# Kernel optimization log

Measured on AMD Instinct MI355X. Metric: run time of the kernel, lower is better.

Reference implementation:

```python
import jax, jax.numpy as jnp
import numpy as np

BATCH = 256
INPUT_DIM = 64
LEVELS = 100
HV_DIM = 10000


def setup_inputs() -> dict:
    key = jax.random.key(0)
    kx, kb = jax.random.split(key)
    x = jax.random.uniform(kx, (BATCH, INPUT_DIM), dtype=jnp.float32)
    base = jax.random.normal(kb, (INPUT_DIM, LEVELS, HV_DIM), dtype=jnp.float32)
    # buffer is L2-normalized along hv_dim at construction time
    base = base / jnp.linalg.norm(base, axis=-1, keepdims=True)
    return {"x": x, "base_hvs": base}


def reference(x, base_hvs):
    D, L, H = base_hvs.shape
    B = x.shape[0]
    xn = jnp.clip(x * (L - 1), 0.0, float(L - 1))          # [B, D]
    lo = jnp.floor(xn).astype(jnp.int32)                    # [B, D]
    hi = jnp.clip(lo + 1, 0, L - 1)                         # [B, D]
    alpha = xn - lo.astype(x.dtype)                         # [B, D]

    def step(acc, inputs):
        bhv, l, h, a = inputs    # bhv: [L, H], l/h/a: [B]
        hv_low = bhv[l]          # [B, H] gather
        hv_high = bhv[h]         # [B, H] gather
        a = a[:, None]
        return acc + (1.0 - a) * hv_low + a * hv_high, None

    init = jnp.zeros((B, H), dtype=x.dtype)
    encoded, _ = jax.lax.scan(step, init, (base_hvs, lo.T, hi.T, alpha.T))
    return encoded / jnp.linalg.norm(encoded, axis=-1, keepdims=True)
```

## Files before the change

### kernel.cpp

```cpp
#include <hip/hip_runtime.h>
#include <hip/hip_fp16.h>
#include <hip/hip_bf16.h>

#define BATCH   256
#define DIMS    64
#define LEVELS  100
#define HVD     10000
#define WH      64
#define NHT     157
#define DSPLIT  8
#define DPER    8
#define TPB     256
#define CHUNK_FLOATS (LEVELS * WH)
#define NSTG    25

typedef unsigned int   uint;
typedef unsigned short ushort;

#define PRM_OFF_BYTES (DSPLIT * BATCH * HVD * 2)

static __device__ __forceinline__ ushort f2bf(float f) {
    __hip_bfloat16 h = __float2bfloat16(f);
    return *reinterpret_cast<ushort*>(&h);
}

__global__ __launch_bounds__(256) void setup_kernel(
    const float* __restrict__ x, uint* __restrict__ prm)
{
    const int i = blockIdx.x * 256 + threadIdx.x;
    if (i >= DIMS * BATCH) return;
    const int d = i >> 8;
    const int b = i & 255;
    float xv = x[b * DIMS + d];
    float xn = fminf(fmaxf(xv * (float)(LEVELS - 1), 0.0f), (float)(LEVELS - 1));
    float fl = floorf(xn);
    int   lo = (int)fl;
    int   hi = lo < LEVELS - 1 ? lo + 1 : LEVELS - 1;
    uint abits = (uint)__half_as_ushort(__float2half(xn - fl));
    prm[i] = abits | ((uint)lo << 16) | ((uint)hi << 24);
}

__global__ __launch_bounds__(TPB, 2) void encode_kernel(
    const float* __restrict__ base,
    const uint* __restrict__ prm,
    ushort*     __restrict__ partial)
{
    __shared__ float s_buf[2][CHUNK_FLOATS];
    __shared__ uint  s_prm[DPER][BATCH];

    const int tid   = threadIdx.x;
    const int w     = tid >> 6;
    const int lane  = tid & 63;
    const int htile = blockIdx.x;
    const int split = blockIdx.y;
    const int h0    = htile * WH;
    const int d0    = split * DPER;
    const int wvalid = (HVD - h0) < WH ? (HVD - h0) : WH;

    {
        const uint4* pg = (const uint4*)(prm + d0 * BATCH);
        uint4* pl = (uint4*)&s_prm[0][0];
        for (int i = tid; i < DPER * BATCH / 4; i += TPB) pl[i] = pg[i];
    }
    __syncthreads();

    const int srow = lane >> 4;
    const int scol = (lane & 15) * 4;
    const float* srcdim = base + (size_t)d0 * LEVELS * HVD + h0;

    auto issue_chunk = [&](int dc, int bufidx) {
        const float* src = srcdim + (size_t)dc * LEVELS * HVD;
        float* dst = &s_buf[bufidx][0];
        for (int p = w; p < NSTG; p += 4) {
            const float* g = src + (size_t)(4 * p + srow) * HVD + scol;
            if (scol < wvalid) {
                __builtin_amdgcn_global_load_lds(
                    (const __attribute__((address_space(1))) uint*)g,
                    (__attribute__((address_space(3))) uint*)(dst + p * 4 * WH),
                    16, 0, 0);
            }
        }
    };

    issue_chunk(0, 0);
    issue_chunk(1, 1);

    const int sub   = lane >> 5;
    const int p2    = lane & 31;
    const int pb    = p2 * 8;
    const int bbase = w * 64;

    float2 acc[32];
    #pragma unroll
    for (int j = 0; j < 32; ++j) acc[j] = make_float2(0.f, 0.f);

    #pragma unroll 1
    for (int dc = 0; dc < DPER; ++dc) {
        if (dc < DPER - 1) asm volatile("s_waitcnt vmcnt(6)" ::: "memory");
        else               asm volatile("s_waitcnt vmcnt(0)" ::: "memory");
        __builtin_amdgcn_s_barrier();

        const char* buf = (const char*)&s_buf[dc & 1][0];
        #pragma unroll
        for (int j = 0; j < 32; ++j) {
            uint2 pp = *(const uint2*)&s_prm[dc][bbase + 2 * j];
            const uint pk = sub ? pp.y : pp.x;
            const float a = __half2float(__ushort_as_half((ushort)(pk & 0xffffu)));
            const int olo = (int)((pk >> 16) & 0xffu) << 8;
            const int ohi = (int)(pk >> 24) << 8;
            const float2 vlo = *(const float2*)(buf + olo + pb);
            const float2 vhi = *(const float2*)(buf + ohi + pb);
            const float wl = 1.0f - a;
            acc[j].x += wl * vlo.x + a * vhi.x;
            acc[j].y += wl * vlo.y + a * vhi.y;
        }
        asm volatile("" ::: "memory");
        __builtin_amdgcn_s_barrier();
        if (dc < DPER - 2) issue_chunk(dc + 2, dc & 1);
    }

    if (p2 * 2 < wvalid) {
        #pragma unroll
        for (int j = 0; j < 32; ++j) {
            const int b = bbase + 2 * j + sub;
            const uint pk = (uint)f2bf(acc[j].x) | ((uint)f2bf(acc[j].y) << 16);
            *(uint*)(partial + ((size_t)split * BATCH + b) * (size_t)HVD + h0 + p2 * 2) = pk;
        }
    }
}

__global__ __launch_bounds__(256) void finish_kernel(
    const ushort* __restrict__ partial,
    float* __restrict__ out)
{
    const int b   = blockIdx.x;
    const int tid = threadIdx.x;

    float ss = 0.f;
    for (int i = tid; i < HVD / 4; i += 256) {
        float4 sum = make_float4(0.f, 0.f, 0.f, 0.f);
        #pragma unroll
        for (int sp = 0; sp < DSPLIT; ++sp) {
            const uint2 u = *(const uint2*)(partial +
                ((size_t)sp * BATCH + b) * (size_t)HVD + i * 4);
            sum.x += __uint_as_float(u.x << 16);
            sum.y += __uint_as_float(u.x & 0xffff0000u);
            sum.z += __uint_as_float(u.y << 16);
            sum.w += __uint_as_float(u.y & 0xffff0000u);
        }
        *(float4*)(out + (size_t)b * HVD + i * 4) = sum;
        ss += sum.x * sum.x + sum.y * sum.y + sum.z * sum.z + sum.w * sum.w;
    }

    __shared__ float red[256];
    red[tid] = ss;
    __syncthreads();
    #pragma unroll
    for (int sh = 128; sh > 0; sh >>= 1) {
        if (tid < sh) red[tid] += red[tid + sh];
        __syncthreads();
    }
    const float inv = rsqrtf(red[0]);

    for (int i = tid; i < HVD / 4; i += 256) {
        float4 v = *(float4*)(out + (size_t)b * HVD + i * 4);
        v.x *= inv; v.y *= inv; v.z *= inv; v.w *= inv;
        *(float4*)(out + (size_t)b * HVD + i * 4) = v;
    }
}

extern "C" void kernel_launch(void* const* d_in, const int* in_sizes, int n_in,
                              void* d_out, int out_size, void* d_ws, size_t ws_size,
                              hipStream_t stream)
{
    const float* x    = (const float*)d_in[0];
    const float* base = (const float*)d_in[1];
    float*       out  = (float*)d_out;
    ushort*      part = (ushort*)d_ws;
    uint*        prm  = (uint*)((char*)d_ws + PRM_OFF_BYTES);

    setup_kernel<<<DIMS, 256, 0, stream>>>(x, prm);
    dim3 grid(NHT, DSPLIT);
    encode_kernel<<<grid, TPB, 0, stream>>>(base, prm, part);
    finish_kernel<<<BATCH, 256, 0, stream>>>(part, out);
}
```

Baseline: 381.4 us.

## Fuse parameter setup into encode kernel and keep finish results in registers

Removes the separate setup kernel: each encode block now computes the lo/hi/alpha parameters for its 8 dims directly from x into shared memory, saving one launch and a global round trip. The finish kernel switches to 1024 threads, each handling 8 elements held in registers, so the output is written once after normalization instead of being written, reread and rewritten. The cost is redundant parameter computation across the 157 h-tiles and a larger reduction tree in finish.

```diff
diff --git a/kernel.cpp b/kernel.cpp
--- a/kernel.cpp
+++ b/kernel.cpp
@@ -11,38 +11,22 @@
 #define DSPLIT  8
 #define DPER    8
 #define TPB     256
+#define FTPB    1024
 #define CHUNK_FLOATS (LEVELS * WH)
 #define NSTG    25
 
 typedef unsigned int   uint;
 typedef unsigned short ushort;
 
-#define PRM_OFF_BYTES (DSPLIT * BATCH * HVD * 2)
 
 static __device__ __forceinline__ ushort f2bf(float f) {
     __hip_bfloat16 h = __float2bfloat16(f);
     return *reinterpret_cast<ushort*>(&h);
 }
 
-__global__ __launch_bounds__(256) void setup_kernel(
-    const float* __restrict__ x, uint* __restrict__ prm)
-{
-    const int i = blockIdx.x * 256 + threadIdx.x;
-    if (i >= DIMS * BATCH) return;
-    const int d = i >> 8;
-    const int b = i & 255;
-    float xv = x[b * DIMS + d];
-    float xn = fminf(fmaxf(xv * (float)(LEVELS - 1), 0.0f), (float)(LEVELS - 1));
-    float fl = floorf(xn);
-    int   lo = (int)fl;
-    int   hi = lo < LEVELS - 1 ? lo + 1 : LEVELS - 1;
-    uint abits = (uint)__half_as_ushort(__float2half(xn - fl));
-    prm[i] = abits | ((uint)lo << 16) | ((uint)hi << 24);
-}
-
 __global__ __launch_bounds__(TPB, 2) void encode_kernel(
+    const float* __restrict__ x,
     const float* __restrict__ base,
-    const uint* __restrict__ prm,
     ushort*     __restrict__ partial)
 {
     __shared__ float s_buf[2][CHUNK_FLOATS];
@@ -58,9 +42,20 @@
     const int wvalid = (HVD - h0) < WH ? (HVD - h0) : WH;
 
     {
-        const uint4* pg = (const uint4*)(prm + d0 * BATCH);
-        uint4* pl = (uint4*)&s_prm[0][0];
-        for (int i = tid; i < DPER * BATCH / 4; i += TPB) pl[i] = pg[i];
+        const float4* xr = (const float4*)(x + (size_t)tid * DIMS + d0);
+        const float4 xa = xr[0];
+        const float4 xb = xr[1];
+        const float xv[8] = { xa.x, xa.y, xa.z, xa.w, xb.x, xb.y, xb.z, xb.w };
+        #pragma unroll
+        for (int k = 0; k < DPER; ++k) {
+            float xn = fminf(fmaxf(xv[k] * (float)(LEVELS - 1), 0.0f),
+                             (float)(LEVELS - 1));
+            float fl = floorf(xn);
+            int   lo = (int)fl;
+            int   hi = lo < LEVELS - 1 ? lo + 1 : LEVELS - 1;
+            uint abits = (uint)__half_as_ushort(__float2half(xn - fl));
+            s_prm[k][tid] = abits | ((uint)lo << 16) | ((uint)hi << 24);
+        }
     }
     __syncthreads();
 
@@ -129,43 +124,60 @@
     }
 }
 
-__global__ __launch_bounds__(256) void finish_kernel(
+__global__ __launch_bounds__(FTPB) void finish_kernel(
     const ushort* __restrict__ partial,
     float* __restrict__ out)
 {
     const int b   = blockIdx.x;
     const int tid = threadIdx.x;
 
-    float ss = 0.f;
-    for (int i = tid; i < HVD / 4; i += 256) {
-        float4 sum = make_float4(0.f, 0.f, 0.f, 0.f);
-        #pragma unroll
-        for (int sp = 0; sp < DSPLIT; ++sp) {
-            const uint2 u = *(const uint2*)(partial +
-                ((size_t)sp * BATCH + b) * (size_t)HVD + i * 4);
-            sum.x += __uint_as_float(u.x << 16);
-            sum.y += __uint_as_float(u.x & 0xffff0000u);
-            sum.z += __uint_as_float(u.y << 16);
-            sum.w += __uint_as_float(u.y & 0xffff0000u);
+    float4 v0[2], v1[2];
+    float  ss = 0.f;
+    #pragma unroll
+    for (int k = 0; k < 2; ++k) {
+        const int g = k * FTPB + tid;
+        float4 a = make_float4(0.f, 0.f, 0.f, 0.f);
+        float4 c = make_float4(0.f, 0.f, 0.f, 0.f);
+        if (g < HVD / 8) {
+            #pragma unroll
+            for (int sp = 0; sp < DSPLIT; ++sp) {
+                const uint4 u = *(const uint4*)(partial +
+                    ((size_t)sp * BATCH + b) * (size_t)HVD + (size_t)g * 8);
+                a.x += __uint_as_float(u.x << 16);
+                a.y += __uint_as_float(u.x & 0xffff0000u);
+                a.z += __uint_as_float(u.y << 16);
+                a.w += __uint_as_float(u.y & 0xffff0000u);
+                c.x += __uint_as_float(u.z << 16);
+                c.y += __uint_as_float(u.z & 0xffff0000u);
+                c.z += __uint_as_float(u.w << 16);
+                c.w += __uint_as_float(u.w & 0xffff0000u);
+            }
+            ss += a.x * a.x + a.y * a.y + a.z * a.z + a.w * a.w
+                + c.x * c.x + c.y * c.y + c.z * c.z + c.w * c.w;
         }
-        *(float4*)(out + (size_t)b * HVD + i * 4) = sum;
-        ss += sum.x * sum.x + sum.y * sum.y + sum.z * sum.z + sum.w * sum.w;
+        v0[k] = a; v1[k] = c;
     }
 
-    __shared__ float red[256];
+    __shared__ float red[FTPB];
     red[tid] = ss;
     __syncthreads();
     #pragma unroll
-    for (int sh = 128; sh > 0; sh >>= 1) {
+    for (int sh = FTPB / 2; sh > 0; sh >>= 1) {
         if (tid < sh) red[tid] += red[tid + sh];
         __syncthreads();
     }
     const float inv = rsqrtf(red[0]);
 
-    for (int i = tid; i < HVD / 4; i += 256) {
-        float4 v = *(float4*)(out + (size_t)b * HVD + i * 4);
-        v.x *= inv; v.y *= inv; v.z *= inv; v.w *= inv;
-        *(float4*)(out + (size_t)b * HVD + i * 4) = v;
+    #pragma unroll
+    for (int k = 0; k < 2; ++k) {
+        const int g = k * FTPB + tid;
+        if (g < HVD / 8) {
+            float4 a = v0[k], c = v1[k];
+            a.x *= inv; a.y *= inv; a.z *= inv; a.w *= inv;
+            c.x *= inv; c.y *= inv; c.z *= inv; c.w *= inv;
+            *(float4*)(out + (size_t)b * HVD + (size_t)g * 8)     = a;
+            *(float4*)(out + (size_t)b * HVD + (size_t)g * 8 + 4) = c;
+        }
     }
 }
 
@@ -177,10 +189,8 @@
     const float* base = (const float*)d_in[1];
     float*       out  = (float*)d_out;
     ushort*      part = (ushort*)d_ws;
-    uint*        prm  = (uint*)((char*)d_ws + PRM_OFF_BYTES);
 
-    setup_kernel<<<DIMS, 256, 0, stream>>>(x, prm);
     dim3 grid(NHT, DSPLIT);
-    encode_kernel<<<grid, TPB, 0, stream>>>(base, prm, part);
-    finish_kernel<<<BATCH, 256, 0, stream>>>(part, out);
+    encode_kernel<<<grid, TPB, 0, stream>>>(x, base, part);
+    finish_kernel<<<BATCH, FTPB, 0, stream>>>(part, out);
 }
```

After: 374.8 us. No clear change (-1.7%).
